# Optimization experiments

Measured on AMD Instinct MI355X. Metric: run time of the kernel, lower is better.

Reference implementation:

```python
import jax, jax.numpy as jnp
import numpy as np

N1, N2, N3 = 262144, 65536, 16384
E1, E2 = 524288, 262144
IN_DIM, HID, HEADS, OUT_DIM = 128, 64, 4, 64
NEG_SLOPE = 0.2   # PyG GATConv default negative_slope
BN_EPS = 1e-5


def setup_inputs() -> dict:
    key = jax.random.key(0)
    ks = jax.random.split(key, 13)
    g = lambda k, shape, scale: jax.random.normal(k, shape, jnp.float32) * scale
    HD = HEADS * HID
    return {
        "x": jax.random.normal(ks[0], (N1, IN_DIM), jnp.float32),
        "W1_src": g(ks[1], (IN_DIM, HD), 1.0 / np.sqrt(IN_DIM)),
        "W1_dst": g(ks[2], (IN_DIM, HD), 1.0 / np.sqrt(IN_DIM)),
        "att1_src": g(ks[3], (HEADS, HID), 1.0 / np.sqrt(HID)),
        "att1_dst": g(ks[4], (HEADS, HID), 1.0 / np.sqrt(HID)),
        "b1": jnp.zeros((HD,), jnp.float32),
        "gamma": jnp.ones((HD,), jnp.float32),
        "beta": jnp.zeros((HD,), jnp.float32),
        "run_mean": jnp.zeros((HD,), jnp.float32),
        "run_var": jnp.ones((HD,), jnp.float32),
        "W2_src": g(ks[5], (HD, OUT_DIM), 1.0 / np.sqrt(HD)),
        "W2_dst": g(ks[6], (HD, OUT_DIM), 1.0 / np.sqrt(HD)),
        "att2_src": g(ks[7], (1, OUT_DIM), 1.0 / np.sqrt(OUT_DIM)),
        "att2_dst": g(ks[8], (1, OUT_DIM), 1.0 / np.sqrt(OUT_DIM)),
        "b2": jnp.zeros((OUT_DIM,), jnp.float32),
        "src1": jax.random.randint(ks[9], (E1,), 0, N1),
        "dst1": jax.random.randint(ks[10], (E1,), 0, N2),
        "src2": jax.random.randint(ks[11], (E2,), 0, N2),
        "dst2": jax.random.randint(ks[12], (E2,), 0, N3),
    }


def gat_conv(x_src, x_dst, W_src, W_dst, att_src, att_dst, bias, src, dst, num_dst, heads, ch):
    """PyG GATConv (bipartite, add_self_loops=False, concat)."""
    h_src = (x_src @ W_src).reshape(-1, heads, ch)   # [N, H, C]
    h_dst = (x_dst @ W_dst).reshape(-1, heads, ch)   # [M, H, C]
    a_src = jnp.sum(h_src * att_src, axis=-1)        # [N, H]
    a_dst = jnp.sum(h_dst * att_dst, axis=-1)        # [M, H]
    e = a_src[src] + a_dst[dst]                      # [E, H] gather
    e = jnp.where(e > 0, e, NEG_SLOPE * e)           # leaky_relu
    # segment softmax over destination nodes
    emax = jax.ops.segment_max(e, dst, num_segments=num_dst)
    emax = jax.lax.stop_gradient(jnp.where(jnp.isfinite(emax), emax, 0.0))
    p = jnp.exp(e - emax[dst])
    denom = jax.ops.segment_sum(p, dst, num_segments=num_dst)
    alpha = p / jnp.maximum(denom[dst], 1e-16)       # [E, H]
    msg = alpha[:, :, None] * h_src[src]             # [E, H, C]
    out = jax.ops.segment_sum(msg, dst, num_segments=num_dst)  # scatter-add
    return out.reshape(num_dst, heads * ch) + bias


def reference(x, W1_src, W1_dst, att1_src, att1_dst, b1, gamma, beta, run_mean, run_var,
              W2_src, W2_dst, att2_src, att2_dst, b2, src1, dst1, src2, dst2):
    # layer 1: GATConv((x, x_target), edge_index) with 4 heads, concat
    h = gat_conv(x, x[:N2], W1_src, W1_dst, att1_src, att1_dst, b1,
                 src1, dst1, N2, HEADS, HID)
    # BatchNorm1d in eval mode (running stats), then ELU; dropout is identity in eval
    h = (h - run_mean) * gamma / jnp.sqrt(run_var + BN_EPS) + beta
    h = jax.nn.elu(h)
    # layer 2: GATConv with heads=1
    out = gat_conv(h, h[:N3], W2_src, W2_dst, att2_src, att2_dst, b2,
                   src2, dst2, N3, 1, OUT_DIM)
    return out
```

## Files before the change

### kernel.cpp

```cpp
#include <hip/hip_runtime.h>


constexpr int N1 = 262144, N2 = 65536, N3 = 16384;
constexpr int E1 = 524288, E2 = 262144;
constexpr int IN_DIM = 128, HID = 64, HEADS = 4, OUT_DIM = 64;
constexpr int HD = HEADS * HID;
constexpr float NEG_SLOPE = 0.2f;
constexpr float BN_EPS = 1e-5f;

typedef __attribute__((ext_vector_type(8))) short bf16x8;
typedef __attribute__((ext_vector_type(8))) unsigned short ushort8;
typedef __attribute__((ext_vector_type(4))) float f32x4;

#define GLOAD_LDS16(gp, lp)                                              \
  __builtin_amdgcn_global_load_lds(                                      \
      (const __attribute__((address_space(1))) unsigned int*)(gp),       \
      (__attribute__((address_space(3))) unsigned int*)(lp), 16, 0, 0)

__device__ inline unsigned short f2bf(float f) {
  unsigned u = __float_as_uint(f);
  u += 0x7FFFu + ((u >> 16) & 1u);
  return (unsigned short)(u >> 16);
}
__device__ inline float bf2f_lo(unsigned v) { return __uint_as_float(v << 16); }
__device__ inline float bf2f_hi(unsigned v) { return __uint_as_float(v & 0xffff0000u); }

__global__ __launch_bounds__(256) void setup_k(
    const float* __restrict__ W1s, const float* __restrict__ W1d,
    const float* __restrict__ A1s, const float* __restrict__ A1d,
    const float* __restrict__ W2s, const float* __restrict__ W2d,
    const float* __restrict__ A2s, const float* __restrict__ A2d,
    const float* __restrict__ b1, const float* __restrict__ gamma,
    const float* __restrict__ beta, const float* __restrict__ mean,
    const float* __restrict__ var,
    float* __restrict__ wa1s, float* __restrict__ wa1d,
    float* __restrict__ wa2s, float* __restrict__ wa2d,
    float* __restrict__ bnsc, float* __restrict__ bnsh,
    int* __restrict__ deg1, int* __restrict__ deg2,
    int* __restrict__ rp1, int* __restrict__ rp2,
    float* __restrict__ a2s, float* __restrict__ a2d,
    unsigned short* __restrict__ w1T, unsigned short* __restrict__ w2T) {
  int b = blockIdx.x, tid = threadIdx.x;
  if (b < 4) {
    int t = b * 256 + tid;
    if (t < HEADS * IN_DIM) {
      int h = t >> 7, k = t & 127;
      float s = 0.f, d = 0.f;
      for (int c = 0; c < HID; ++c) {
        s += W1s[k * HD + h * HID + c] * A1s[h * HID + c];
        d += W1d[k * HD + h * HID + c] * A1d[h * HID + c];
      }
      wa1s[t] = s; wa1d[t] = d;
    } else if (t < HEADS * IN_DIM + HD) {
      int k = t - HEADS * IN_DIM;
      float s = 0.f, d = 0.f;
      for (int c = 0; c < OUT_DIM; ++c) {
        s += W2s[k * OUT_DIM + c] * A2s[c];
        d += W2d[k * OUT_DIM + c] * A2d[c];
      }
      wa2s[k] = s; wa2d[k] = d;
    } else if (t < HEADS * IN_DIM + 2 * HD) {
      int c = t - HEADS * IN_DIM - HD;
      float sc = gamma[c] * rsqrtf(var[c] + BN_EPS);
      bnsc[c] = sc;
      bnsh[c] = beta[c] + (b1[c] - mean[c]) * sc;
    }
  } else if (b < 68) {
    int i = (b - 4) * 256 + tid;
    int stride = 64 * 256;
    for (int j = i; j < N2; j += stride) { deg1[j] = 0; a2s[j] = 0.f; }
    for (int j = i; j < N3; j += stride) { deg2[j] = 0; a2d[j] = 0.f; }
    if (i == 0) { rp1[0] = 0; rp2[0] = 0; }
  } else if (b < 84) {
    int t = (b - 68) * 256 + tid;
    int n = t >> 4, g = t & 15;
    ushort8 o;
#pragma unroll
    for (int j = 0; j < 8; ++j) o[j] = f2bf(W1s[(size_t)(g * 8 + j) * HD + n]);
    *reinterpret_cast<ushort8*>(w1T + (size_t)n * IN_DIM + (size_t)(g ^ (n & 7)) * 8) = o;
  } else {
    int t = (b - 84) * 256 + tid;
    int n = t >> 5, G = t & 31;
    int k0 = G * 8;
    ushort8 o;
#pragma unroll
    for (int j = 0; j < 8; ++j) o[j] = f2bf(W2s[(size_t)(k0 + j) * OUT_DIM + n]);
    int idx = ((k0 >> 7) << 7) + ((k0 & 127) ^ ((n & 7) << 3));
    *reinterpret_cast<ushort8*>(w2T + (size_t)n * HD + idx) = o;
  }
}

__global__ __launch_bounds__(256) void hist12_k(
    const int* __restrict__ dst1, int* __restrict__ deg1, int* __restrict__ rank1,
    const int* __restrict__ dst2, int* __restrict__ deg2, int* __restrict__ rank2) {
  int b = blockIdx.x;
  if (b < E1 / 256) {
    int i = b * 256 + threadIdx.x;
    rank1[i] = atomicAdd(&deg1[dst1[i]], 1);
  } else {
    int i = (b - E1 / 256) * 256 + threadIdx.x;
    rank2[i] = atomicAdd(&deg2[dst2[i]], 1);
  }
}

__device__ inline void scan_body(const int* in, int* out, int* bsums, int b) {
  __shared__ int s[256];
  int tid = threadIdx.x;
  int i0 = b * 1024 + tid * 4;
  int x0 = in[i0], x1 = in[i0 + 1], x2 = in[i0 + 2], x3 = in[i0 + 3];
  int t = x0 + x1 + x2 + x3;
  s[tid] = t;
  __syncthreads();
  for (int off = 1; off < 256; off <<= 1) {
    int v = (tid >= off) ? s[tid - off] : 0;
    __syncthreads();
    s[tid] += v;
    __syncthreads();
  }
  int base = s[tid] - t;
  out[i0] = base + x0;
  out[i0 + 1] = base + x0 + x1;
  out[i0 + 2] = base + x0 + x1 + x2;
  out[i0 + 3] = base + t;
  if (tid == 255) bsums[b] = s[255];
}

__global__ __launch_bounds__(256) void scanA_k(
    const int* __restrict__ deg1, int* __restrict__ o1, int* __restrict__ bs1,
    const int* __restrict__ deg2, int* __restrict__ o2, int* __restrict__ bs2) {
  int b = blockIdx.x;
  if (b < 64) scan_body(deg1, o1, bs1, b);
  else scan_body(deg2, o2, bs2, b - 64);
}

__global__ __launch_bounds__(256) void scanC_k(
    int* __restrict__ o1, const int* __restrict__ bs1,
    int* __restrict__ o2, const int* __restrict__ bs2) {
  __shared__ int sadd;
  int b = blockIdx.x;
  int* out; const int* bs; int bb;
  if (b < 64) { out = o1; bs = bs1; bb = b; }
  else { out = o2; bs = bs2; bb = b - 64; }
  int tid = threadIdx.x;
  if (tid < 64) {
    int v = (tid < bb) ? bs[tid] : 0;
#pragma unroll
    for (int off = 32; off; off >>= 1) v += __shfl_xor(v, off, 64);
    if (tid == 0) sadd = v;
  }
  __syncthreads();
  if (bb == 0) return;
  int add = sadd;
  int i0 = bb * 1024 + tid * 4;
  out[i0] += add; out[i0 + 1] += add; out[i0 + 2] += add; out[i0 + 3] += add;
}

__global__ __launch_bounds__(256) void conv_scores1(
    const float* __restrict__ x, const float* __restrict__ wa_s,
    const float* __restrict__ wa_d, unsigned short* __restrict__ xbf,
    float* __restrict__ a_src, float* __restrict__ a_dst) {
  __shared__ float ws[HEADS * IN_DIM], wd[HEADS * IN_DIM];
  int tid = threadIdx.x;
  for (int i = tid; i < HEADS * IN_DIM; i += 256) { ws[i] = wa_s[i]; wd[i] = wa_d[i]; }
  __syncthreads();
  int row = blockIdx.x * 16 + (tid >> 4);
  int g = tid & 15;
  float4 v0 = *reinterpret_cast<const float4*>(x + (size_t)row * IN_DIM + g * 8);
  float4 v1 = *reinterpret_cast<const float4*>(x + (size_t)row * IN_DIM + g * 8 + 4);
  float xv[8] = {v0.x, v0.y, v0.z, v0.w, v1.x, v1.y, v1.z, v1.w};
  ushort8 o;
#pragma unroll
  for (int j = 0; j < 8; ++j) o[j] = f2bf(xv[j]);
  *reinterpret_cast<ushort8*>(xbf + (size_t)row * IN_DIM + g * 8) = o;
#pragma unroll
  for (int h = 0; h < HEADS; ++h) {
    float p = 0.f;
#pragma unroll
    for (int j = 0; j < 8; ++j) p = fmaf(xv[j], ws[h * IN_DIM + g * 8 + j], p);
#pragma unroll
    for (int off = 1; off < 16; off <<= 1) p += __shfl_xor(p, off, 64);
    if (g == 0) a_src[(size_t)row * HEADS + h] = p;
  }
  if (row < N2) {
#pragma unroll
    for (int h = 0; h < HEADS; ++h) {
      float p = 0.f;
#pragma unroll
      for (int j = 0; j < 8; ++j) p = fmaf(xv[j], wd[h * IN_DIM + g * 8 + j], p);
#pragma unroll
      for (int off = 1; off < 16; off <<= 1) p += __shfl_xor(p, off, 64);
      if (g == 0) a_dst[(size_t)row * HEADS + h] = p;
    }
  }
}

__global__ __launch_bounds__(256) void scatter1p_k(
    const int* __restrict__ src, const int* __restrict__ dst,
    const int* __restrict__ rp, const int* __restrict__ rank,
    const float* __restrict__ a1s, const float* __restrict__ a1d,
    int* __restrict__ srcs, float4* __restrict__ pexp) {
  int i = blockIdx.x * 256 + threadIdx.x;
  int s = src[i], d = dst[i];
  float4 as = *reinterpret_cast<const float4*>(a1s + (size_t)s * HEADS);
  float4 ad = *reinterpret_cast<const float4*>(a1d + (size_t)d * HEADS);
  float4 p;
#pragma unroll
  for (int h = 0; h < 4; ++h) {
    float e = ((const float*)&as)[h] + ((const float*)&ad)[h];
    e = e > 0.f ? e : NEG_SLOPE * e;
    ((float*)&p)[h] = __expf(e);
  }
  int pos = rp[d] + rank[i];
  srcs[pos] = s;
  pexp[pos] = p;
}

__global__ __launch_bounds__(256) void agg1x(
    const int* __restrict__ rp, const int* __restrict__ srcs,
    const float4* __restrict__ pexp, const unsigned short* __restrict__ xbf,
    unsigned short* __restrict__ z) {
  int d = blockIdx.x * 4 + (threadIdx.x >> 6);
  int lane = threadIdx.x & 63;
  int beg = rp[d], end = rp[d + 1];
  float z0[4] = {0.f, 0.f, 0.f, 0.f}, z1[4] = {0.f, 0.f, 0.f, 0.f};
  float ss[4] = {0.f, 0.f, 0.f, 0.f}, ss2[4] = {0.f, 0.f, 0.f, 0.f};
  int j = beg;
  for (; j + 2 <= end; j += 2) {
    int s0 = srcs[j], s1 = srcs[j + 1];
    float4 p0 = pexp[j], p1 = pexp[j + 1];
    unsigned u0 = ((const unsigned*)(xbf + (size_t)s0 * IN_DIM))[lane];
    unsigned u1 = ((const unsigned*)(xbf + (size_t)s1 * IN_DIM))[lane];
    float v0x = bf2f_lo(u0), v0y = bf2f_hi(u0);
    float v1x = bf2f_lo(u1), v1y = bf2f_hi(u1);
#pragma unroll
    for (int h = 0; h < 4; ++h) {
      float ph0 = ((const float*)&p0)[h], ph1 = ((const float*)&p1)[h];
      z0[h] = fmaf(ph0, v0x, fmaf(ph1, v1x, z0[h]));
      z1[h] = fmaf(ph0, v0y, fmaf(ph1, v1y, z1[h]));
      ss[h] += ph0; ss2[h] += ph1;
    }
  }
  if (j < end) {
    int s0 = srcs[j];
    float4 p0 = pexp[j];
    unsigned u0 = ((const unsigned*)(xbf + (size_t)s0 * IN_DIM))[lane];
    float v0x = bf2f_lo(u0), v0y = bf2f_hi(u0);
#pragma unroll
    for (int h = 0; h < 4; ++h) {
      float ph0 = ((const float*)&p0)[h];
      z0[h] = fmaf(ph0, v0x, z0[h]);
      z1[h] = fmaf(ph0, v0y, z1[h]);
      ss[h] += ph0;
    }
  }
  int G = lane >> 2;
  int idx = ((G ^ (d & 7)) << 3) + ((lane & 3) << 1);
#pragma unroll
  for (int h = 0; h < 4; ++h) {
    float inv = 1.f / fmaxf(ss[h] + ss2[h], 1e-30f);
    unsigned out = (unsigned)f2bf(z0[h] * inv) | ((unsigned)f2bf(z1[h] * inv) << 16);
    *reinterpret_cast<unsigned*>(z + ((size_t)h * N2 + d) * IN_DIM + idx) = out;
  }
}

__global__ __launch_bounds__(256) void finalize1(
    const unsigned short* __restrict__ z, const unsigned short* __restrict__ w1T,
    const float* __restrict__ bnsc, const float* __restrict__ bnsh,
    const float* __restrict__ wa2s, const float* __restrict__ wa2d,
    unsigned short* __restrict__ acc1, float* __restrict__ a2s,
    float* __restrict__ a2d) {
  __shared__ char sm[49152];
  const int tid = threadIdx.x, wave = tid >> 6, lane = tid & 63;
  const int row0 = blockIdx.x * 128;
  const int h = blockIdx.y;
  const char* gA = (const char*)(z + ((size_t)h * N2 + row0) * IN_DIM);
  const char* gB = (const char*)(w1T + (size_t)h * 64 * IN_DIM);
#pragma unroll
  for (int it = 0; it < 8; ++it) {
    int off = it * 4096 + wave * 1024 + lane * 16;
    GLOAD_LDS16(gA + off, sm + off);
  }
#pragma unroll
  for (int it = 0; it < 4; ++it) {
    int off = it * 4096 + wave * 1024 + lane * 16;
    GLOAD_LDS16(gB + off, sm + 32768 + off);
  }
  __syncthreads();
  const int rbase = wave * 32;
  const int kl = (lane >> 4) * 8, fr = lane & 15;
  f32x4 acc[2][4] = {};
#pragma unroll
  for (int ks = 0; ks < 4; ++ks) {
    int k0 = ks * 32 + kl;
    bf16x8 a[2], b[4];
#pragma unroll
    for (int i = 0; i < 2; ++i) {
      int ra = rbase + i * 16 + fr;
      a[i] = *reinterpret_cast<const bf16x8*>(
          sm + ((size_t)ra * 128 + (k0 ^ ((ra & 7) << 3))) * 2);
    }
#pragma unroll
    for (int jj = 0; jj < 4; ++jj) {
      int cb = jj * 16 + fr;
      b[jj] = *reinterpret_cast<const bf16x8*>(
          sm + 32768 + ((size_t)cb * 128 + (k0 ^ ((cb & 7) << 3))) * 2);
    }
#pragma unroll
    for (int i = 0; i < 2; ++i)
#pragma unroll
      for (int jj = 0; jj < 4; ++jj)
        acc[i][jj] = __builtin_amdgcn_mfma_f32_16x16x32_bf16(a[i], b[jj], acc[i][jj], 0, 0, 0);
  }
  float sc[4], sh[4], w2sv[4], w2dv[4];
#pragma unroll
  for (int jj = 0; jj < 4; ++jj) {
    int c = h * 64 + jj * 16 + fr;
    sc[jj] = bnsc[c]; sh[jj] = bnsh[c]; w2sv[jj] = wa2s[c]; w2dv[jj] = wa2d[c];
  }
  const int g = lane >> 4;
#pragma unroll
  for (int i = 0; i < 2; ++i) {
#pragma unroll
    for (int q = 0; q < 4; ++q) {
      int row = row0 + rbase + i * 16 + g * 4 + q;
      float s2s = 0.f, s2d = 0.f;
#pragma unroll
      for (int jj = 0; jj < 4; ++jj) {
        float v = acc[i][jj][q] * sc[jj] + sh[jj];
        v = v > 0.f ? v : expm1f(v);
        s2s = fmaf(v, w2sv[jj], s2s);
        s2d = fmaf(v, w2dv[jj], s2d);
        int c = h * 64 + jj * 16 + fr;
        int idx = ((c >> 7) << 7) + ((c & 127) ^ ((row & 7) << 3));
        acc1[(size_t)row * HD + idx] = f2bf(v);
      }
#pragma unroll
      for (int off = 1; off < 16; off <<= 1) {
        s2s += __shfl_xor(s2s, off, 64);
        s2d += __shfl_xor(s2d, off, 64);
      }
      if (fr == 0) {
        atomicAdd(&a2s[row], s2s);
        if (row < N3) atomicAdd(&a2d[row], s2d);
      }
    }
  }
}

__global__ __launch_bounds__(256) void scatter2p_k(
    const int* __restrict__ src, const int* __restrict__ dst,
    const int* __restrict__ rp, const int* __restrict__ rank,
    const float* __restrict__ a2s, const float* __restrict__ a2d,
    int* __restrict__ srcs, float* __restrict__ pexp) {
  int i = blockIdx.x * 256 + threadIdx.x;
  int s = src[i], d = dst[i];
  float e = a2s[s] + a2d[d];
  e = e > 0.f ? e : NEG_SLOPE * e;
  int pos = rp[d] + rank[i];
  srcs[pos] = s;
  pexp[pos] = __expf(e);
}

__global__ __launch_bounds__(256) void gemm2(
    const unsigned short* __restrict__ acc1, const unsigned short* __restrict__ w2T,
    unsigned short* __restrict__ h2bf) {
  __shared__ char sm[65536];
  const int tid = threadIdx.x, wave = tid >> 6, lane = tid & 63;
  const int row0 = blockIdx.x * 128;
  const char* gB = (const char*)w2T;
#pragma unroll
  for (int it = 0; it < 8; ++it) {
    int off = it * 4096 + wave * 1024 + lane * 16;
    GLOAD_LDS16(gB + off, sm + 32768 + off);
  }
  const int rbase = wave * 32;
  const int kl = (lane >> 4) * 8, fr = lane & 15;
  f32x4 acc[2][4] = {};
  for (int kh = 0; kh < 2; ++kh) {
    __syncthreads();
#pragma unroll
    for (int it = 0; it < 8; ++it) {
      int r = it * 16 + (tid >> 4);
      const char* srcp = (const char*)(acc1 + (size_t)(row0 + r) * HD) +
                         kh * 256 + (tid & 15) * 16;
      GLOAD_LDS16(srcp, sm + it * 4096 + tid * 16);
    }
    __syncthreads();
#pragma unroll
    for (int ks = 0; ks < 4; ++ks) {
      int k0 = ks * 32 + kl;
      bf16x8 a[2], b[4];
#pragma unroll
      for (int i = 0; i < 2; ++i) {
        int ra = rbase + i * 16 + fr;
        a[i] = *reinterpret_cast<const bf16x8*>(
            sm + ((size_t)ra * 128 + (k0 ^ ((ra & 7) << 3))) * 2);
      }
#pragma unroll
      for (int jj = 0; jj < 4; ++jj) {
        int cb = jj * 16 + fr;
        b[jj] = *reinterpret_cast<const bf16x8*>(
            sm + 32768 + ((size_t)cb * 256 + kh * 128 + (k0 ^ ((cb & 7) << 3))) * 2);
      }
#pragma unroll
      for (int i = 0; i < 2; ++i)
#pragma unroll
        for (int jj = 0; jj < 4; ++jj)
          acc[i][jj] = __builtin_amdgcn_mfma_f32_16x16x32_bf16(a[i], b[jj], acc[i][jj], 0, 0, 0);
    }
  }
  const int g = lane >> 4;
#pragma unroll
  for (int i = 0; i < 2; ++i)
#pragma unroll
    for (int q = 0; q < 4; ++q) {
      int row = row0 + rbase + i * 16 + g * 4 + q;
#pragma unroll
      for (int jj = 0; jj < 4; ++jj)
        h2bf[(size_t)row * OUT_DIM + jj * 16 + fr] = f2bf(acc[i][jj][q]);
    }
}

__global__ __launch_bounds__(256) void agg2(
    const int* __restrict__ rp, const int* __restrict__ srcs,
    const float* __restrict__ pe, const unsigned short* __restrict__ h2bf,
    const float* __restrict__ b2, float* __restrict__ out) {
  int d = blockIdx.x * 4 + (threadIdx.x >> 6);
  int lane = threadIdx.x & 63;
  int beg = rp[d], end = rp[d + 1];
  float ssum = 0.f, ssum2 = 0.f, acc = 0.f, acc2 = 0.f;
  int j = beg;
  for (; j + 2 <= end; j += 2) {
    int s0 = srcs[j], s1 = srcs[j + 1];
    float p0 = pe[j], p1 = pe[j + 1];
    float v0 = __uint_as_float((unsigned)h2bf[(size_t)s0 * OUT_DIM + lane] << 16);
    float v1 = __uint_as_float((unsigned)h2bf[(size_t)s1 * OUT_DIM + lane] << 16);
    acc = fmaf(p0, v0, acc); acc2 = fmaf(p1, v1, acc2);
    ssum += p0; ssum2 += p1;
  }
  if (j < end) {
    int s0 = srcs[j];
    float p0 = pe[j];
    float v0 = __uint_as_float((unsigned)h2bf[(size_t)s0 * OUT_DIM + lane] << 16);
    acc = fmaf(p0, v0, acc);
    ssum += p0;
  }
  acc += acc2; ssum += ssum2;
  out[(size_t)d * OUT_DIM + lane] = acc / fmaxf(ssum, 1e-30f) + b2[lane];
}

extern "C" void kernel_launch(void* const* d_in, const int* in_sizes, int n_in,
                              void* d_out, int out_size, void* d_ws, size_t ws_size,
                              hipStream_t stream) {
  const float* x     = (const float*)d_in[0];
  const float* W1s   = (const float*)d_in[1];
  const float* W1d   = (const float*)d_in[2];
  const float* A1s   = (const float*)d_in[3];
  const float* A1d   = (const float*)d_in[4];
  const float* b1    = (const float*)d_in[5];
  const float* gamma = (const float*)d_in[6];
  const float* beta  = (const float*)d_in[7];
  const float* rmean = (const float*)d_in[8];
  const float* rvar  = (const float*)d_in[9];
  const float* W2s   = (const float*)d_in[10];
  const float* W2d   = (const float*)d_in[11];
  const float* A2s   = (const float*)d_in[12];
  const float* A2d   = (const float*)d_in[13];
  const float* b2    = (const float*)d_in[14];
  const int* src1    = (const int*)d_in[15];
  const int* dst1    = (const int*)d_in[16];
  const int* src2    = (const int*)d_in[17];
  const int* dst2    = (const int*)d_in[18];
  (void)in_sizes; (void)n_in; (void)out_size; (void)ws_size;

  char* W = (char*)d_ws;
  size_t off = 0;
  auto alloc = [&](size_t bytes) { void* p = W + off; off = (off + bytes + 255) & ~(size_t)255; return p; };
  unsigned short* xbf  = (unsigned short*)alloc((size_t)N1 * IN_DIM * 2);
  unsigned short* z    = (unsigned short*)alloc((size_t)HEADS * N2 * IN_DIM * 2);
  unsigned short* w1T  = (unsigned short*)alloc((size_t)HD * IN_DIM * 2);
  unsigned short* w2T  = (unsigned short*)alloc((size_t)OUT_DIM * HD * 2);
  unsigned short* acc1 = (unsigned short*)alloc((size_t)N2 * HD * 2);
  unsigned short* h2bf = (unsigned short*)alloc((size_t)N2 * OUT_DIM * 2);
  float* a1s   = (float*)alloc((size_t)N1 * HEADS * 4);
  float* a1d   = (float*)alloc((size_t)N2 * HEADS * 4);
  float* a2s   = (float*)alloc((size_t)N2 * 4);
  float* a2d   = (float*)alloc((size_t)N3 * 4);
  float4* pexp1 = (float4*)alloc((size_t)E1 * 16);
  float* pexp2 = (float*)alloc((size_t)E2 * 4);
  int* deg1    = (int*)alloc((size_t)N2 * 4);
  int* rank1   = (int*)alloc((size_t)E1 * 4);
  int* rp1     = (int*)alloc((size_t)(N2 + 1) * 4);
  int* srcs1   = (int*)alloc((size_t)E1 * 4);
  int* deg2    = (int*)alloc((size_t)N3 * 4);
  int* rank2   = (int*)alloc((size_t)E2 * 4);
  int* rp2     = (int*)alloc((size_t)(N3 + 1) * 4);
  int* srcs2   = (int*)alloc((size_t)E2 * 4);
  float* wa1s  = (float*)alloc(HEADS * IN_DIM * 4);
  float* wa1d  = (float*)alloc(HEADS * IN_DIM * 4);
  float* wa2s  = (float*)alloc(HD * 4);
  float* wa2d  = (float*)alloc(HD * 4);
  float* bnsc  = (float*)alloc(HD * 4);
  float* bnsh  = (float*)alloc(HD * 4);
  int* bsums1  = (int*)alloc(64 * 4);
  int* bsums2  = (int*)alloc(64 * 4);

  setup_k<<<92, 256, 0, stream>>>(W1s, W1d, A1s, A1d, W2s, W2d, A2s, A2d,
                                  b1, gamma, beta, rmean, rvar,
                                  wa1s, wa1d, wa2s, wa2d, bnsc, bnsh,
                                  deg1, deg2, rp1, rp2, a2s, a2d, w1T, w2T);
  hist12_k<<<E1 / 256 + E2 / 256, 256, 0, stream>>>(dst1, deg1, rank1,
                                                    dst2, deg2, rank2);
  scanA_k<<<80, 256, 0, stream>>>(deg1, rp1 + 1, bsums1, deg2, rp2 + 1, bsums2);
  scanC_k<<<80, 256, 0, stream>>>(rp1 + 1, bsums1, rp2 + 1, bsums2);

  conv_scores1<<<N1 / 16, 256, 0, stream>>>(x, wa1s, wa1d, xbf, a1s, a1d);
  scatter1p_k<<<E1 / 256, 256, 0, stream>>>(src1, dst1, rp1, rank1, a1s, a1d,
                                            srcs1, pexp1);
  agg1x<<<N2 / 4, 256, 0, stream>>>(rp1, srcs1, pexp1, xbf, z);
  finalize1<<<dim3(N2 / 128, HEADS), 256, 0, stream>>>(
      z, w1T, bnsc, bnsh, wa2s, wa2d, acc1, a2s, a2d);

  scatter2p_k<<<E2 / 256, 256, 0, stream>>>(src2, dst2, rp2, rank2, a2s, a2d,
                                            srcs2, pexp2);
  gemm2<<<N2 / 128, 256, 0, stream>>>(acc1, w2T, h2bf);
  agg2<<<N3 / 4, 256, 0, stream>>>(rp2, srcs2, pexp2, h2bf, b2, (float*)d_out);
}
```

Measured before the change: 424.1 us.

## Fuse layer-1 finalize with layer-2 GEMM and gather fp32 x directly

The separate finalize1 and gemm2 kernels are merged into one kernel. Each 128-row block loops over all four heads, keeps the BN+ELU activations in LDS, then multiplies them by W2 in place, so the acc1 intermediate never goes through global memory. The bf16 copy of x is also dropped: agg1x now gathers fp32 x rows, which removes a write pass over x but doubles the bytes read per gathered row. The fused kernel launches only 512 blocks with 112KB of LDS each, which lowers occupancy and parallelism.

Result: no change. 424.5 us (+0.1%).

```diff
diff --git a/kernel.cpp b/kernel.cpp
--- a/kernel.cpp
+++ b/kernel.cpp
@@ -22,8 +22,6 @@
   u += 0x7FFFu + ((u >> 16) & 1u);
   return (unsigned short)(u >> 16);
 }
-__device__ inline float bf2f_lo(unsigned v) { return __uint_as_float(v << 16); }
-__device__ inline float bf2f_hi(unsigned v) { return __uint_as_float(v & 0xffff0000u); }
 
 __global__ __launch_bounds__(256) void setup_k(
     const float* __restrict__ W1s, const float* __restrict__ W1d,
@@ -157,8 +155,8 @@
 
 __global__ __launch_bounds__(256) void conv_scores1(
     const float* __restrict__ x, const float* __restrict__ wa_s,
-    const float* __restrict__ wa_d, unsigned short* __restrict__ xbf,
-    float* __restrict__ a_src, float* __restrict__ a_dst) {
+    const float* __restrict__ wa_d, float* __restrict__ a_src,
+    float* __restrict__ a_dst) {
   __shared__ float ws[HEADS * IN_DIM], wd[HEADS * IN_DIM];
   int tid = threadIdx.x;
   for (int i = tid; i < HEADS * IN_DIM; i += 256) { ws[i] = wa_s[i]; wd[i] = wa_d[i]; }
@@ -168,10 +166,6 @@
   float4 v0 = *reinterpret_cast<const float4*>(x + (size_t)row * IN_DIM + g * 8);
   float4 v1 = *reinterpret_cast<const float4*>(x + (size_t)row * IN_DIM + g * 8 + 4);
   float xv[8] = {v0.x, v0.y, v0.z, v0.w, v1.x, v1.y, v1.z, v1.w};
-  ushort8 o;
-#pragma unroll
-  for (int j = 0; j < 8; ++j) o[j] = f2bf(xv[j]);
-  *reinterpret_cast<ushort8*>(xbf + (size_t)row * IN_DIM + g * 8) = o;
 #pragma unroll
   for (int h = 0; h < HEADS; ++h) {
     float p = 0.f;
@@ -217,7 +211,7 @@
 
 __global__ __launch_bounds__(256) void agg1x(
     const int* __restrict__ rp, const int* __restrict__ srcs,
-    const float4* __restrict__ pexp, const unsigned short* __restrict__ xbf,
+    const float4* __restrict__ pexp, const float* __restrict__ x,
     unsigned short* __restrict__ z) {
   int d = blockIdx.x * 4 + (threadIdx.x >> 6);
   int lane = threadIdx.x & 63;
@@ -228,28 +222,25 @@
   for (; j + 2 <= end; j += 2) {
     int s0 = srcs[j], s1 = srcs[j + 1];
     float4 p0 = pexp[j], p1 = pexp[j + 1];
-    unsigned u0 = ((const unsigned*)(xbf + (size_t)s0 * IN_DIM))[lane];
-    unsigned u1 = ((const unsigned*)(xbf + (size_t)s1 * IN_DIM))[lane];
-    float v0x = bf2f_lo(u0), v0y = bf2f_hi(u0);
-    float v1x = bf2f_lo(u1), v1y = bf2f_hi(u1);
+    float2 v0 = *reinterpret_cast<const float2*>(x + (size_t)s0 * IN_DIM + lane * 2);
+    float2 v1 = *reinterpret_cast<const float2*>(x + (size_t)s1 * IN_DIM + lane * 2);
 #pragma unroll
     for (int h = 0; h < 4; ++h) {
       float ph0 = ((const float*)&p0)[h], ph1 = ((const float*)&p1)[h];
-      z0[h] = fmaf(ph0, v0x, fmaf(ph1, v1x, z0[h]));
-      z1[h] = fmaf(ph0, v0y, fmaf(ph1, v1y, z1[h]));
+      z0[h] = fmaf(ph0, v0.x, fmaf(ph1, v1.x, z0[h]));
+      z1[h] = fmaf(ph0, v0.y, fmaf(ph1, v1.y, z1[h]));
       ss[h] += ph0; ss2[h] += ph1;
     }
   }
   if (j < end) {
     int s0 = srcs[j];
     float4 p0 = pexp[j];
-    unsigned u0 = ((const unsigned*)(xbf + (size_t)s0 * IN_DIM))[lane];
-    float v0x = bf2f_lo(u0), v0y = bf2f_hi(u0);
+    float2 v0 = *reinterpret_cast<const float2*>(x + (size_t)s0 * IN_DIM + lane * 2);
 #pragma unroll
     for (int h = 0; h < 4; ++h) {
       float ph0 = ((const float*)&p0)[h];
-      z0[h] = fmaf(ph0, v0x, z0[h]);
-      z1[h] = fmaf(ph0, v0y, z1[h]);
+      z0[h] = fmaf(ph0, v0.x, z0[h]);
+      z1[h] = fmaf(ph0, v0.y, z1[h]);
       ss[h] += ph0;
     }
   }
@@ -263,88 +254,141 @@
   }
 }
 
-__global__ __launch_bounds__(256) void finalize1(
+__global__ __launch_bounds__(256) void fin2_k(
     const unsigned short* __restrict__ z, const unsigned short* __restrict__ w1T,
+    const unsigned short* __restrict__ w2T,
     const float* __restrict__ bnsc, const float* __restrict__ bnsh,
     const float* __restrict__ wa2s, const float* __restrict__ wa2d,
-    unsigned short* __restrict__ acc1, float* __restrict__ a2s,
-    float* __restrict__ a2d) {
-  __shared__ char sm[49152];
+    float* __restrict__ a2s, float* __restrict__ a2d,
+    unsigned short* __restrict__ h2bf) {
+  extern __shared__ char sm[];
+  char* vbuf = sm + 49152;
   const int tid = threadIdx.x, wave = tid >> 6, lane = tid & 63;
   const int row0 = blockIdx.x * 128;
-  const int h = blockIdx.y;
-  const char* gA = (const char*)(z + ((size_t)h * N2 + row0) * IN_DIM);
-  const char* gB = (const char*)(w1T + (size_t)h * 64 * IN_DIM);
+  const int rbase = wave * 32;
+  const int kl = (lane >> 4) * 8, fr = lane & 15, g = lane >> 4;
+  float s2s_acc[2][4] = {{0.f, 0.f, 0.f, 0.f}, {0.f, 0.f, 0.f, 0.f}};
+  float s2d_acc[2][4] = {{0.f, 0.f, 0.f, 0.f}, {0.f, 0.f, 0.f, 0.f}};
+
+  for (int h = 0; h < 4; ++h) {
+    const char* gA = (const char*)(z + ((size_t)h * N2 + row0) * IN_DIM);
+    const char* gB = (const char*)(w1T + (size_t)h * 64 * IN_DIM);
+#pragma unroll
+    for (int it = 0; it < 8; ++it) {
+      int off = it * 4096 + wave * 1024 + lane * 16;
+      GLOAD_LDS16(gA + off, sm + off);
+    }
+#pragma unroll
+    for (int it = 0; it < 4; ++it) {
+      int off = it * 4096 + wave * 1024 + lane * 16;
+      GLOAD_LDS16(gB + off, sm + 32768 + off);
+    }
+    __syncthreads();
+    f32x4 acc[2][4] = {};
+#pragma unroll
+    for (int ks = 0; ks < 4; ++ks) {
+      int k0 = ks * 32 + kl;
+      bf16x8 a[2], b[4];
+#pragma unroll
+      for (int i = 0; i < 2; ++i) {
+        int ra = rbase + i * 16 + fr;
+        a[i] = *reinterpret_cast<const bf16x8*>(
+            sm + ((size_t)ra * 128 + (k0 ^ ((ra & 7) << 3))) * 2);
+      }
+#pragma unroll
+      for (int jj = 0; jj < 4; ++jj) {
+        int cb = jj * 16 + fr;
+        b[jj] = *reinterpret_cast<const bf16x8*>(
+            sm + 32768 + ((size_t)cb * 128 + (k0 ^ ((cb & 7) << 3))) * 2);
+      }
+#pragma unroll
+      for (int i = 0; i < 2; ++i)
+#pragma unroll
+        for (int jj = 0; jj < 4; ++jj)
+          acc[i][jj] = __builtin_amdgcn_mfma_f32_16x16x32_bf16(a[i], b[jj], acc[i][jj], 0, 0, 0);
+    }
+    float sc[4], sh[4], w2sv[4], w2dv[4];
+#pragma unroll
+    for (int jj = 0; jj < 4; ++jj) {
+      int c = h * 64 + jj * 16 + fr;
+      sc[jj] = bnsc[c]; sh[jj] = bnsh[c]; w2sv[jj] = wa2s[c]; w2dv[jj] = wa2d[c];
+    }
+#pragma unroll
+    for (int i = 0; i < 2; ++i)
+#pragma unroll
+      for (int q = 0; q < 4; ++q) {
+        int rl = rbase + i * 16 + g * 4 + q;
+#pragma unroll
+        for (int jj = 0; jj < 4; ++jj) {
+          float v = acc[i][jj][q] * sc[jj] + sh[jj];
+          v = v > 0.f ? v : expm1f(v);
+          s2s_acc[i][q] = fmaf(v, w2sv[jj], s2s_acc[i][q]);
+          s2d_acc[i][q] = fmaf(v, w2dv[jj], s2d_acc[i][q]);
+          int c = h * 64 + jj * 16 + fr;
+          int idx = ((c >> 7) << 7) + ((c & 127) ^ ((rl & 7) << 3));
+          *reinterpret_cast<unsigned short*>(vbuf + ((size_t)rl * 256 + idx) * 2) = f2bf(v);
+        }
+      }
+    __syncthreads();
+  }
+
 #pragma unroll
   for (int it = 0; it < 8; ++it) {
     int off = it * 4096 + wave * 1024 + lane * 16;
-    GLOAD_LDS16(gA + off, sm + off);
-  }
-#pragma unroll
-  for (int it = 0; it < 4; ++it) {
-    int off = it * 4096 + wave * 1024 + lane * 16;
-    GLOAD_LDS16(gB + off, sm + 32768 + off);
-  }
-  __syncthreads();
-  const int rbase = wave * 32;
-  const int kl = (lane >> 4) * 8, fr = lane & 15;
-  f32x4 acc[2][4] = {};
-#pragma unroll
-  for (int ks = 0; ks < 4; ++ks) {
-    int k0 = ks * 32 + kl;
-    bf16x8 a[2], b[4];
-#pragma unroll
-    for (int i = 0; i < 2; ++i) {
-      int ra = rbase + i * 16 + fr;
-      a[i] = *reinterpret_cast<const bf16x8*>(
-          sm + ((size_t)ra * 128 + (k0 ^ ((ra & 7) << 3))) * 2);
-    }
-#pragma unroll
-    for (int jj = 0; jj < 4; ++jj) {
-      int cb = jj * 16 + fr;
-      b[jj] = *reinterpret_cast<const bf16x8*>(
-          sm + 32768 + ((size_t)cb * 128 + (k0 ^ ((cb & 7) << 3))) * 2);
-    }
-#pragma unroll
-    for (int i = 0; i < 2; ++i)
-#pragma unroll
-      for (int jj = 0; jj < 4; ++jj)
-        acc[i][jj] = __builtin_amdgcn_mfma_f32_16x16x32_bf16(a[i], b[jj], acc[i][jj], 0, 0, 0);
-  }
-  float sc[4], sh[4], w2sv[4], w2dv[4];
-#pragma unroll
-  for (int jj = 0; jj < 4; ++jj) {
-    int c = h * 64 + jj * 16 + fr;
-    sc[jj] = bnsc[c]; sh[jj] = bnsh[c]; w2sv[jj] = wa2s[c]; w2dv[jj] = wa2d[c];
-  }
-  const int g = lane >> 4;
-#pragma unroll
-  for (int i = 0; i < 2; ++i) {
+    GLOAD_LDS16((const char*)w2T + off, sm + off);
+  }
+#pragma unroll
+  for (int i = 0; i < 2; ++i)
 #pragma unroll
     for (int q = 0; q < 4; ++q) {
-      int row = row0 + rbase + i * 16 + g * 4 + q;
-      float s2s = 0.f, s2d = 0.f;
-#pragma unroll
-      for (int jj = 0; jj < 4; ++jj) {
-        float v = acc[i][jj][q] * sc[jj] + sh[jj];
-        v = v > 0.f ? v : expm1f(v);
-        s2s = fmaf(v, w2sv[jj], s2s);
-        s2d = fmaf(v, w2dv[jj], s2d);
-        int c = h * 64 + jj * 16 + fr;
-        int idx = ((c >> 7) << 7) + ((c & 127) ^ ((row & 7) << 3));
-        acc1[(size_t)row * HD + idx] = f2bf(v);
-      }
+      float s2s = s2s_acc[i][q], s2d = s2d_acc[i][q];
 #pragma unroll
       for (int off = 1; off < 16; off <<= 1) {
         s2s += __shfl_xor(s2s, off, 64);
         s2d += __shfl_xor(s2d, off, 64);
       }
       if (fr == 0) {
+        int row = row0 + rbase + i * 16 + g * 4 + q;
         atomicAdd(&a2s[row], s2s);
         if (row < N3) atomicAdd(&a2d[row], s2d);
       }
     }
-  }
+  __syncthreads();
+
+  f32x4 acc2[2][4] = {};
+#pragma unroll
+  for (int kh = 0; kh < 2; ++kh)
+#pragma unroll
+    for (int ks = 0; ks < 4; ++ks) {
+      int k0 = ks * 32 + kl;
+      bf16x8 a[2], b[4];
+#pragma unroll
+      for (int i = 0; i < 2; ++i) {
+        int ra = rbase + i * 16 + fr;
+        a[i] = *reinterpret_cast<const bf16x8*>(
+            vbuf + ((size_t)ra * 256 + kh * 128 + (k0 ^ ((ra & 7) << 3))) * 2);
+      }
+#pragma unroll
+      for (int jj = 0; jj < 4; ++jj) {
+        int cb = jj * 16 + fr;
+        b[jj] = *reinterpret_cast<const bf16x8*>(
+            sm + ((size_t)cb * 256 + kh * 128 + (k0 ^ ((cb & 7) << 3))) * 2);
+      }
+#pragma unroll
+      for (int i = 0; i < 2; ++i)
+#pragma unroll
+        for (int jj = 0; jj < 4; ++jj)
+          acc2[i][jj] = __builtin_amdgcn_mfma_f32_16x16x32_bf16(a[i], b[jj], acc2[i][jj], 0, 0, 0);
+    }
+#pragma unroll
+  for (int i = 0; i < 2; ++i)
+#pragma unroll
+    for (int q = 0; q < 4; ++q) {
+      int row = row0 + rbase + i * 16 + g * 4 + q;
+#pragma unroll
+      for (int jj = 0; jj < 4; ++jj)
+        h2bf[(size_t)row * OUT_DIM + jj * 16 + fr] = f2bf(acc2[i][jj][q]);
+    }
 }
 
 __global__ __launch_bounds__(256) void scatter2p_k(
@@ -359,66 +403,6 @@
   int pos = rp[d] + rank[i];
   srcs[pos] = s;
   pexp[pos] = __expf(e);
-}
-
-__global__ __launch_bounds__(256) void gemm2(
-    const unsigned short* __restrict__ acc1, const unsigned short* __restrict__ w2T,
-    unsigned short* __restrict__ h2bf) {
-  __shared__ char sm[65536];
-  const int tid = threadIdx.x, wave = tid >> 6, lane = tid & 63;
-  const int row0 = blockIdx.x * 128;
-  const char* gB = (const char*)w2T;
-#pragma unroll
-  for (int it = 0; it < 8; ++it) {
-    int off = it * 4096 + wave * 1024 + lane * 16;
-    GLOAD_LDS16(gB + off, sm + 32768 + off);
-  }
-  const int rbase = wave * 32;
-  const int kl = (lane >> 4) * 8, fr = lane & 15;
-  f32x4 acc[2][4] = {};
-  for (int kh = 0; kh < 2; ++kh) {
-    __syncthreads();
-#pragma unroll
-    for (int it = 0; it < 8; ++it) {
-      int r = it * 16 + (tid >> 4);
-      const char* srcp = (const char*)(acc1 + (size_t)(row0 + r) * HD) +
-                         kh * 256 + (tid & 15) * 16;
-      GLOAD_LDS16(srcp, sm + it * 4096 + tid * 16);
-    }
-    __syncthreads();
-#pragma unroll
-    for (int ks = 0; ks < 4; ++ks) {
-      int k0 = ks * 32 + kl;
-      bf16x8 a[2], b[4];
-#pragma unroll
-      for (int i = 0; i < 2; ++i) {
-        int ra = rbase + i * 16 + fr;
-        a[i] = *reinterpret_cast<const bf16x8*>(
-            sm + ((size_t)ra * 128 + (k0 ^ ((ra & 7) << 3))) * 2);
-      }
-#pragma unroll
-      for (int jj = 0; jj < 4; ++jj) {
-        int cb = jj * 16 + fr;
-        b[jj] = *reinterpret_cast<const bf16x8*>(
-            sm + 32768 + ((size_t)cb * 256 + kh * 128 + (k0 ^ ((cb & 7) << 3))) * 2);
-      }
-#pragma unroll
-      for (int i = 0; i < 2; ++i)
-#pragma unroll
-        for (int jj = 0; jj < 4; ++jj)
-          acc[i][jj] = __builtin_amdgcn_mfma_f32_16x16x32_bf16(a[i], b[jj], acc[i][jj], 0, 0, 0);
-    }
-  }
-  const int g = lane >> 4;
-#pragma unroll
-  for (int i = 0; i < 2; ++i)
-#pragma unroll
-    for (int q = 0; q < 4; ++q) {
-      int row = row0 + rbase + i * 16 + g * 4 + q;
-#pragma unroll
-      for (int jj = 0; jj < 4; ++jj)
-        h2bf[(size_t)row * OUT_DIM + jj * 16 + fr] = f2bf(acc[i][jj][q]);
-    }
 }
 
 __global__ __launch_bounds__(256) void agg2(
@@ -476,11 +460,9 @@
   char* W = (char*)d_ws;
   size_t off = 0;
   auto alloc = [&](size_t bytes) { void* p = W + off; off = (off + bytes + 255) & ~(size_t)255; return p; };
-  unsigned short* xbf  = (unsigned short*)alloc((size_t)N1 * IN_DIM * 2);
   unsigned short* z    = (unsigned short*)alloc((size_t)HEADS * N2 * IN_DIM * 2);
   unsigned short* w1T  = (unsigned short*)alloc((size_t)HD * IN_DIM * 2);
   unsigned short* w2T  = (unsigned short*)alloc((size_t)OUT_DIM * HD * 2);
-  unsigned short* acc1 = (unsigned short*)alloc((size_t)N2 * HD * 2);
   unsigned short* h2bf = (unsigned short*)alloc((size_t)N2 * OUT_DIM * 2);
   float* a1s   = (float*)alloc((size_t)N1 * HEADS * 4);
   float* a1d   = (float*)alloc((size_t)N2 * HEADS * 4);
@@ -514,15 +496,14 @@
   scanA_k<<<80, 256, 0, stream>>>(deg1, rp1 + 1, bsums1, deg2, rp2 + 1, bsums2);
   scanC_k<<<80, 256, 0, stream>>>(rp1 + 1, bsums1, rp2 + 1, bsums2);
 
-  conv_scores1<<<N1 / 16, 256, 0, stream>>>(x, wa1s, wa1d, xbf, a1s, a1d);
+  conv_scores1<<<N1 / 16, 256, 0, stream>>>(x, wa1s, wa1d, a1s, a1d);
   scatter1p_k<<<E1 / 256, 256, 0, stream>>>(src1, dst1, rp1, rank1, a1s, a1d,
                                             srcs1, pexp1);
-  agg1x<<<N2 / 4, 256, 0, stream>>>(rp1, srcs1, pexp1, xbf, z);
-  finalize1<<<dim3(N2 / 128, HEADS), 256, 0, stream>>>(
-      z, w1T, bnsc, bnsh, wa2s, wa2d, acc1, a2s, a2d);
+  agg1x<<<N2 / 4, 256, 0, stream>>>(rp1, srcs1, pexp1, x, z);
+  fin2_k<<<N2 / 128, 256, 114688, stream>>>(z, w1T, w2T, bnsc, bnsh,
+                                            wa2s, wa2d, a2s, a2d, h2bf);
 
   scatter2p_k<<<E2 / 256, 256, 0, stream>>>(src2, dst2, rp2, rank2, a2s, a2d,
                                             srcs2, pexp2);
-  gemm2<<<N2 / 128, 256, 0, stream>>>(acc1, w2T, h2bf);
   agg2<<<N3 / 4, 256, 0, stream>>>(rp2, srcs2, pexp2, h2bf, b2, (float*)d_out);
 }
```
